# Performance work log

Hardware: AMD Instinct MI355X
Metric: run time of the kernel (lower is better)

The kernel has to match this reference:

```python
import jax, jax.numpy as jnp
import numpy as np

N = 100000      # nodes
E = 1600000     # edges
DIN = 128       # input features
H = 64          # hidden size of each of the 3 GATConv layers
EPS = 1e-16     # PyG softmax denominator epsilon


def _glorot(key, shape):
    fan_in, fan_out = shape[0], shape[-1]
    s = float(np.sqrt(6.0 / (fan_in + fan_out)))
    return jax.random.uniform(key, shape, jnp.float32, -s, s)


def setup_inputs() -> dict:
    key = jax.random.key(0)
    ks = jax.random.split(key, 18)
    x = jax.random.normal(ks[0], (N, DIN), jnp.float32)
    edge_index = jax.random.randint(ks[1], (2, E), 0, N, jnp.int32)
    dims = [(DIN, H), (H, H), (H, H)]
    params = {}
    ki = 2
    for li, (din, dout) in enumerate(dims, start=1):
        params[f"W{li}s"] = _glorot(ks[ki], (din, dout)); ki += 1
        params[f"W{li}d"] = _glorot(ks[ki], (din, dout)); ki += 1
        params[f"a{li}s"] = _glorot(ks[ki], (1, dout))[0]; ki += 1
        params[f"a{li}d"] = _glorot(ks[ki], (1, dout))[0]; ki += 1
        params[f"b{li}"] = jnp.zeros((dout,), jnp.float32)
    return dict(x=x, edge_index=edge_index, **params)


def gat_layer(x, src, dst, Ws, Wd, a_s, a_d, b):
    # single-head GATConv, negative_slope=0 -> relu on logits, no self-loops
    hs = x @ Ws                      # [N, H] source-side features (messages)
    hd = x @ Wd                      # [N, H] destination-side features
    als = hs @ a_s                   # [N] per-node source attention term
    ald = hd @ a_d                   # [N] per-node destination attention term
    logit = jax.nn.relu(als[src] + ald[dst])          # [E]
    # segment softmax over incoming edges of each destination node
    seg_max = jax.ops.segment_max(logit, dst, num_segments=N)
    ex = jnp.exp(logit - seg_max[dst])                # [E]
    denom = jax.ops.segment_sum(ex, dst, num_segments=N)
    alpha = ex / (denom[dst] + EPS)                   # [E]
    out = jax.ops.segment_sum(alpha[:, None] * hs[src], dst, num_segments=N)
    return out + b


def reference(x, edge_index,
              W1s, W1d, a1s, a1d, b1,
              W2s, W2d, a2s, a2d, b2,
              W3s, W3d, a3s, a3d, b3):
    src, dst = edge_index[0], edge_index[1]
    x = gat_layer(x, src, dst, W1s, W1d, a1s, a1d, b1)
    x = gat_layer(x, src, dst, W2s, W2d, a2s, a2d, b2)
    x = gat_layer(x, src, dst, W3s, W3d, a3s, a3d, b3)
    return x
```

## Files before the change

kernel.cpp:

```cpp
#include <hip/hip_runtime.h>
#include <hip/hip_fp16.h>

#define HDIM 64
#define EPS_F 1e-16f
#define CH 8192
#define BSH 9
#define SRCB 17

__global__ void compute_vd_all_kernel(const float* __restrict__ Wd1, const float* __restrict__ ad1,
                                      const float* __restrict__ Wd2, const float* __restrict__ ad2,
                                      const float* __restrict__ Wd3, const float* __restrict__ ad3,
                                      float* __restrict__ vd) {
    int l = blockIdx.x;
    int k = threadIdx.x;
    const float* Wd = (l == 0) ? Wd1 : (l == 1) ? Wd2 : Wd3;
    const float* ad = (l == 0) ? ad1 : (l == 1) ? ad2 : ad3;
    int din = (l == 0) ? 128 : 64;
    int off = (l == 0) ? 0 : (l == 1) ? 128 : 192;
    if (k >= din) return;
    float s = 0.f;
#pragma unroll
    for (int j = 0; j < HDIM; ++j) s = fmaf(Wd[k * HDIM + j], ad[j], s);
    vd[off + k] = s;
}

template <int DIN>
__global__ __launch_bounds__(256) void gemm_fused_kernel(
    const float* __restrict__ xin, const float* __restrict__ Ws,
    const float* __restrict__ as_, const float* __restrict__ vd,
    __half* __restrict__ hs, float* __restrict__ als, float* __restrict__ ald,
    int N) {
    __shared__ float wsh[DIN * HDIM];
    __shared__ float xs[32 * (DIN + 4)];
    __shared__ float ash[HDIM];
    __shared__ float vdsh[DIN];

    const int tid = threadIdx.x;
    const int n0 = blockIdx.x * 32;

    for (int i = tid * 4; i < DIN * HDIM; i += 256 * 4)
        *(float4*)&wsh[i] = *(const float4*)&Ws[i];
    if (tid < HDIM) ash[tid] = as_[tid];
    if (tid < DIN) vdsh[tid] = vd[tid];
    for (int i = tid; i < 32 * DIN / 4; i += 256) {
        int idx = i * 4;
        int n = idx / DIN, k = idx - n * DIN;
        float4 v = make_float4(0.f, 0.f, 0.f, 0.f);
        if (n0 + n < N) v = *(const float4*)&xin[(size_t)(n0 + n) * DIN + k];
        *(float4*)&xs[n * (DIN + 4) + k] = v;
    }
    __syncthreads();

    const int nl = tid >> 3, jg = tid & 7, j0 = jg * 8;
    const int n = n0 + nl;
    float acc[8] = {0.f, 0.f, 0.f, 0.f, 0.f, 0.f, 0.f, 0.f};
    float aldp = 0.f;
    const float* xrow = &xs[nl * (DIN + 4)];
#pragma unroll 4
    for (int k = 0; k < DIN; ++k) {
        float xv = xrow[k];
        aldp = fmaf(xv, vdsh[k], aldp);
        float4 w0 = *(const float4*)&wsh[k * HDIM + j0];
        float4 w1 = *(const float4*)&wsh[k * HDIM + j0 + 4];
        acc[0] = fmaf(xv, w0.x, acc[0]);
        acc[1] = fmaf(xv, w0.y, acc[1]);
        acc[2] = fmaf(xv, w0.z, acc[2]);
        acc[3] = fmaf(xv, w0.w, acc[3]);
        acc[4] = fmaf(xv, w1.x, acc[4]);
        acc[5] = fmaf(xv, w1.y, acc[5]);
        acc[6] = fmaf(xv, w1.z, acc[6]);
        acc[7] = fmaf(xv, w1.w, acc[7]);
    }
    float alsp = 0.f;
#pragma unroll
    for (int jj = 0; jj < 8; ++jj) alsp = fmaf(acc[jj], ash[j0 + jj], alsp);
    alsp += __shfl_down(alsp, 4, 8);
    alsp += __shfl_down(alsp, 2, 8);
    alsp += __shfl_down(alsp, 1, 8);

    if (n < N) {
        union { __half h[8]; float4 f; } u;
#pragma unroll
        for (int jj = 0; jj < 8; ++jj) u.h[jj] = __float2half_rn(acc[jj]);
        *(float4*)&hs[(size_t)n * HDIM + j0] = u.f;
        if (jg == 0) {
            als[n] = alsp;
            ald[n] = aldp;
        }
    }
}

__global__ void zero_kernel(int* __restrict__ p, int n) {
    int i = blockIdx.x * blockDim.x + threadIdx.x;
    if (i < n) p[i] = 0;
}

__global__ __launch_bounds__(256) void bucket_hist_kernel(const int* __restrict__ dst,
                                                          int* __restrict__ gbucket, int E) {
    __shared__ int bh[256];
    int t = threadIdx.x;
    bh[t] = 0;
    __syncthreads();
    int e0 = blockIdx.x * CH;
#pragma unroll
    for (int i = 0; i < CH / 256; ++i) {
        int e = e0 + i * 256 + t;
        if (e < E) atomicAdd(&bh[dst[e] >> BSH], 1);
    }
    __syncthreads();
    if (bh[t]) atomicAdd(&gbucket[t], bh[t]);
}

__global__ __launch_bounds__(256) void bucket_scan_kernel(const int* __restrict__ gbucket,
                                                          int* __restrict__ bucket_base,
                                                          int* __restrict__ bucket_cur,
                                                          int nbuk, int E) {
    __shared__ int tmp[256];
    int t = threadIdx.x;
    int v = (t < nbuk) ? gbucket[t] : 0;
    tmp[t] = v;
    __syncthreads();
    for (int off = 1; off < 256; off <<= 1) {
        int a = (t >= off) ? tmp[t - off] : 0;
        __syncthreads();
        tmp[t] += a;
        __syncthreads();
    }
    int excl = tmp[t] - v;
    if (t < nbuk) {
        bucket_base[t] = excl;
        bucket_cur[t] = excl;
    }
    if (t == 0) bucket_base[nbuk] = E;
}

__global__ __launch_bounds__(256) void bin_kernel(const int* __restrict__ src,
                                                  const int* __restrict__ dst,
                                                  int* __restrict__ bucket_cur,
                                                  unsigned int* __restrict__ epack, int E) {
    __shared__ int lcnt[256], lbase[256];
    int t = threadIdx.x;
    int e0 = blockIdx.x * CH;
    lcnt[t] = 0;
    __syncthreads();
#pragma unroll
    for (int i = 0; i < CH / 256; ++i) {
        int e = e0 + i * 256 + t;
        if (e < E) atomicAdd(&lcnt[dst[e] >> BSH], 1);
    }
    __syncthreads();
    int c = lcnt[t];
    if (c) lbase[t] = atomicAdd(&bucket_cur[t], c);
    __syncthreads();
    lcnt[t] = 0;
    __syncthreads();
#pragma unroll
    for (int i = 0; i < CH / 256; ++i) {
        int e = e0 + i * 256 + t;
        if (e < E) {
            int d = dst[e];
            int bk = d >> BSH;
            int pos = lbase[bk] + atomicAdd(&lcnt[bk], 1);
            epack[pos] = ((unsigned int)(d & 511) << SRCB) | (unsigned int)src[e];
        }
    }
}

__global__ __launch_bounds__(256) void bucket_sort_kernel(
    const unsigned int* __restrict__ epack, const int* __restrict__ bucket_base,
    int* __restrict__ rowptr, int* __restrict__ csr_src, int N, int E) {
    __shared__ int cnt[512], cur[512], psum[256];
    int b = blockIdx.x, t = threadIdx.x;
    int n0 = b << BSH;
    int nlocal = min(512, N - n0);
    int bstart = bucket_base[b], bend = bucket_base[b + 1];
    cnt[t] = 0;
    cnt[t + 256] = 0;
    __syncthreads();
    for (int k = bstart + t; k < bend; k += 256)
        atomicAdd(&cnt[epack[k] >> SRCB], 1);
    __syncthreads();
    int p = cnt[2 * t] + cnt[2 * t + 1];
    psum[t] = p;
    __syncthreads();
    for (int off = 1; off < 256; off <<= 1) {
        int a = (t >= off) ? psum[t - off] : 0;
        __syncthreads();
        psum[t] += a;
        __syncthreads();
    }
    int excl = psum[t] - p;
    int o0 = excl, o1 = excl + cnt[2 * t];
    cur[2 * t] = o0;
    cur[2 * t + 1] = o1;
    if (2 * t < nlocal) rowptr[n0 + 2 * t] = bstart + o0;
    if (2 * t + 1 < nlocal) rowptr[n0 + 2 * t + 1] = bstart + o1;
    __syncthreads();
    for (int k = bstart + t; k < bend; k += 256) {
        unsigned int e = epack[k];
        int pos = bstart + atomicAdd(&cur[e >> SRCB], 1);
        csr_src[pos] = (int)(e & ((1u << SRCB) - 1u));
    }
    if (b == 0 && t == 0) rowptr[N] = E;
}

__global__ __launch_bounds__(256) void gat_sparse_kernel(
    const int* __restrict__ rowptr, const int* __restrict__ csr_src,
    const float* __restrict__ als, const float* __restrict__ ald,
    const __half* __restrict__ hs, const float* __restrict__ b,
    float* __restrict__ out, int N) {
    int wid = (blockIdx.x * 256 + threadIdx.x) >> 6;
    int lane = threadIdx.x & 63;
    if (wid >= N) return;
    int start = rowptr[wid], end = rowptr[wid + 1];
    int deg = end - start;
    float aldd = ald[wid];

    if (deg <= 64) {
        bool valid = lane < deg;
        int s = 0;
        float ex = 0.f;
        if (valid) {
            s = csr_src[start + lane];
            float l = als[s] + aldd;
            l = l > 0.f ? l : 0.f;
            ex = __expf(l);
        }
        float denom = ex;
#pragma unroll
        for (int off = 32; off; off >>= 1) denom += __shfl_xor(denom, off);

        const int esub = lane >> 4, fg = lane & 15;
        float a0 = 0.f, a1 = 0.f, a2 = 0.f, a3 = 0.f;
        for (int k0 = 0; k0 < deg; k0 += 8) {
            int ia = k0 + esub, ib = k0 + 4 + esub;
            float exa = __shfl(ex, ia), exb = __shfl(ex, ib);
            int sa = __shfl(s, ia), sb = __shfl(s, ib);
            union { uint2 u; __half h[4]; } ra, rb;
            ra.u = *(const uint2*)&hs[(size_t)sa * HDIM + fg * 4];
            rb.u = *(const uint2*)&hs[(size_t)sb * HDIM + fg * 4];
            a0 = fmaf(exa, __half2float(ra.h[0]), a0);
            a1 = fmaf(exa, __half2float(ra.h[1]), a1);
            a2 = fmaf(exa, __half2float(ra.h[2]), a2);
            a3 = fmaf(exa, __half2float(ra.h[3]), a3);
            a0 = fmaf(exb, __half2float(rb.h[0]), a0);
            a1 = fmaf(exb, __half2float(rb.h[1]), a1);
            a2 = fmaf(exb, __half2float(rb.h[2]), a2);
            a3 = fmaf(exb, __half2float(rb.h[3]), a3);
        }
#pragma unroll
        for (int off = 16; off < 64; off <<= 1) {
            a0 += __shfl_xor(a0, off);
            a1 += __shfl_xor(a1, off);
            a2 += __shfl_xor(a2, off);
            a3 += __shfl_xor(a3, off);
        }
        if (esub == 0) {
            float inv = 1.f / (denom + EPS_F);
            const float4 b4 = *(const float4*)&b[fg * 4];
            float4 o;
            o.x = a0 * inv + b4.x;
            o.y = a1 * inv + b4.y;
            o.z = a2 * inv + b4.z;
            o.w = a3 * inv + b4.w;
            *(float4*)&out[(size_t)wid * HDIM + fg * 4] = o;
        }
        return;
    }

    float m = 0.f;
    for (int k = start + lane; k < end; k += 64)
        m = fmaxf(m, als[csr_src[k]] + aldd);
#pragma unroll
    for (int off = 32; off; off >>= 1) m = fmaxf(m, __shfl_xor(m, off));

    const int esub = lane >> 4, fg = lane & 15;
    float4 acc = make_float4(0.f, 0.f, 0.f, 0.f);
    float denom = 0.f;
    for (int k0 = start; k0 < end; k0 += 8) {
        int ka = k0 + esub, kb = k0 + 4 + esub;
        float exa = 0.f, exb = 0.f;
        uint2 ra = make_uint2(0u, 0u), rb = make_uint2(0u, 0u);
        if (ka < end) {
            int s = csr_src[ka];
            float l = als[s] + aldd;
            l = l > 0.f ? l : 0.f;
            exa = __expf(l - m);
            ra = *(const uint2*)&hs[(size_t)s * HDIM + fg * 4];
        }
        if (kb < end) {
            int s = csr_src[kb];
            float l = als[s] + aldd;
            l = l > 0.f ? l : 0.f;
            exb = __expf(l - m);
            rb = *(const uint2*)&hs[(size_t)s * HDIM + fg * 4];
        }
        denom += exa + exb;
        float2 fa0 = __half22float2(*(__half2*)&ra.x);
        float2 fa1 = __half22float2(*(__half2*)&ra.y);
        float2 fb0 = __half22float2(*(__half2*)&rb.x);
        float2 fb1 = __half22float2(*(__half2*)&rb.y);
        acc.x = fmaf(exa, fa0.x, acc.x);
        acc.y = fmaf(exa, fa0.y, acc.y);
        acc.z = fmaf(exa, fa1.x, acc.z);
        acc.w = fmaf(exa, fa1.y, acc.w);
        acc.x = fmaf(exb, fb0.x, acc.x);
        acc.y = fmaf(exb, fb0.y, acc.y);
        acc.z = fmaf(exb, fb1.x, acc.z);
        acc.w = fmaf(exb, fb1.y, acc.w);
    }
#pragma unroll
    for (int off = 16; off < 64; off <<= 1) {
        acc.x += __shfl_xor(acc.x, off);
        acc.y += __shfl_xor(acc.y, off);
        acc.z += __shfl_xor(acc.z, off);
        acc.w += __shfl_xor(acc.w, off);
        denom += __shfl_xor(denom, off);
    }
    if (esub == 0) {
        float inv = 1.f / (denom + EPS_F);
        const float4 b4 = *(const float4*)&b[fg * 4];
        float4 o;
        o.x = acc.x * inv + b4.x;
        o.y = acc.y * inv + b4.y;
        o.z = acc.z * inv + b4.z;
        o.w = acc.w * inv + b4.w;
        *(float4*)&out[(size_t)wid * HDIM + fg * 4] = o;
    }
}

extern "C" void kernel_launch(void* const* d_in, const int* in_sizes, int n_in,
                              void* d_out, int out_size, void* d_ws, size_t ws_size,
                              hipStream_t stream) {
    const float* x = (const float*)d_in[0];
    const int* ei = (const int*)d_in[1];
    const int E = in_sizes[1] / 2;
    const int din1 = in_sizes[2] / HDIM;
    const int N = in_sizes[0] / din1;
    const int* src = ei;
    const int* dst = ei + E;

    const float* P[15];
    for (int i = 0; i < 15; ++i) P[i] = (const float*)d_in[2 + i];

    float* w = (float*)d_ws;
    __half* hs = (__half*)w;  w += (size_t)N * HDIM / 2;
    float* xb = w;            w += (size_t)N * HDIM;
    float* als = w;           w += N;
    float* ald = w;           w += N;
    float* vd = w;            w += 256;
    int* ip = (int*)w;
    unsigned int* epack = (unsigned int*)ip; ip += E;
    int* csr_src = ip;        ip += E;
    int* rowptr = ip;         ip += N + 1;
    int* gbucket = ip;        ip += 256;
    int* bucket_base = ip;    ip += 257;
    int* bucket_cur = ip;     ip += 256;

    const int BT = 256;
    const int gridN32 = (N + 31) / 32;
    const int nbuk = (N + 511) >> BSH;
    const int gridCH = (E + CH - 1) / CH;
    const int gridSparse = (N * 64 + BT - 1) / BT;

    zero_kernel<<<1, 256, 0, stream>>>(gbucket, 256);
    bucket_hist_kernel<<<gridCH, BT, 0, stream>>>(dst, gbucket, E);
    bucket_scan_kernel<<<1, BT, 0, stream>>>(gbucket, bucket_base, bucket_cur, nbuk, E);
    bin_kernel<<<gridCH, BT, 0, stream>>>(src, dst, bucket_cur, epack, E);
    bucket_sort_kernel<<<nbuk, BT, 0, stream>>>(epack, bucket_base, rowptr, csr_src, N, E);

    compute_vd_all_kernel<<<3, 128, 0, stream>>>(P[1], P[3], P[6], P[8], P[11], P[13], vd);

    auto run_layer = [&](const float* xin, int din, const float* Ws, const float* vdl,
                         const float* as_, const float* b, float* xout) {
        if (din == 128)
            gemm_fused_kernel<128><<<gridN32, BT, 0, stream>>>(xin, Ws, as_, vdl, hs, als, ald, N);
        else
            gemm_fused_kernel<64><<<gridN32, BT, 0, stream>>>(xin, Ws, as_, vdl, hs, als, ald, N);
        gat_sparse_kernel<<<gridSparse, BT, 0, stream>>>(rowptr, csr_src, als, ald, hs, b,
                                                         xout, N);
    };

    float* out = (float*)d_out;
    run_layer(x,   din1, P[0],  vd,       P[2],  P[4],  xb);
    run_layer(xb,  HDIM, P[5],  vd + 128, P[7],  P[9],  out);
    run_layer(out, HDIM, P[10], vd + 192, P[12], P[14], out);
}
```

Baseline: 414.4 us.

## Use MFMA fp16 GEMM with fused attention columns and fp16 intermediate activations

The scalar FP32 dense projection is replaced by an MFMA 16x16x32 fp16 kernel. Its weight matrix is pre-transposed and gets two extra columns, Ws·a_s and Wd·a_d, so the per-node attention terms come out of the same matrix multiply. Shared memory uses XOR swizzling, and layers 1 and 2 now write hidden activations as fp16, which halves their write and read traffic. This lowers dense compute and memory cost, at the price of fp16 rounding on the inputs, the attention vectors and the intermediate activations.

```diff
diff --git a/kernel.cpp b/kernel.cpp
--- a/kernel.cpp
+++ b/kernel.cpp
@@ -7,85 +7,128 @@
 #define BSH 9
 #define SRCB 17
 
-__global__ void compute_vd_all_kernel(const float* __restrict__ Wd1, const float* __restrict__ ad1,
-                                      const float* __restrict__ Wd2, const float* __restrict__ ad2,
-                                      const float* __restrict__ Wd3, const float* __restrict__ ad3,
-                                      float* __restrict__ vd) {
-    int l = blockIdx.x;
-    int k = threadIdx.x;
-    const float* Wd = (l == 0) ? Wd1 : (l == 1) ? Wd2 : Wd3;
-    const float* ad = (l == 0) ? ad1 : (l == 1) ? ad2 : ad3;
-    int din = (l == 0) ? 128 : 64;
-    int off = (l == 0) ? 0 : (l == 1) ? 128 : 192;
-    if (k >= din) return;
-    float s = 0.f;
-#pragma unroll
-    for (int j = 0; j < HDIM; ++j) s = fmaf(Wd[k * HDIM + j], ad[j], s);
-    vd[off + k] = s;
-}
-
-template <int DIN>
-__global__ __launch_bounds__(256) void gemm_fused_kernel(
-    const float* __restrict__ xin, const float* __restrict__ Ws,
-    const float* __restrict__ as_, const float* __restrict__ vd,
-    __half* __restrict__ hs, float* __restrict__ als, float* __restrict__ ald,
-    int N) {
-    __shared__ float wsh[DIN * HDIM];
-    __shared__ float xs[32 * (DIN + 4)];
-    __shared__ float ash[HDIM];
-    __shared__ float vdsh[DIN];
-
+using half8  = __attribute__((ext_vector_type(8))) _Float16;
+using floatx4 = __attribute__((ext_vector_type(4))) float;
+
+__global__ void build_wt_kernel(const float* __restrict__ Ws, const float* __restrict__ as_,
+                                const float* __restrict__ Wd, const float* __restrict__ ad,
+                                _Float16* __restrict__ wt, int din) {
+    int tid = threadIdx.x;
+    for (int idx = tid; idx < 64 * din; idx += 256) {
+        int c = idx / din, k = idx - c * din;
+        wt[c * din + k] = (_Float16)Ws[k * 64 + c];
+    }
+    for (int k = tid; k < din; k += 256) {
+        float u = 0.f, v = 0.f;
+#pragma unroll
+        for (int j = 0; j < 64; ++j) {
+            u = fmaf(Ws[k * 64 + j], as_[j], u);
+            v = fmaf(Wd[k * 64 + j], ad[j], v);
+        }
+        wt[64 * din + k] = (_Float16)u;
+        wt[65 * din + k] = (_Float16)v;
+    }
+    for (int idx = tid; idx < 14 * din; idx += 256) wt[66 * din + idx] = (_Float16)0.f;
+}
+
+template <int DIN, bool F32IN>
+__global__ __launch_bounds__(256) void gemm_mfma_kernel(
+    const void* __restrict__ xin, const _Float16* __restrict__ wt,
+    _Float16* __restrict__ hs, float* __restrict__ als, float* __restrict__ ald, int N) {
+    constexpr int KB = DIN / 8;
+    __shared__ _Float16 xs[64 * DIN];
+    __shared__ _Float16 ws[80 * DIN];
     const int tid = threadIdx.x;
-    const int n0 = blockIdx.x * 32;
-
-    for (int i = tid * 4; i < DIN * HDIM; i += 256 * 4)
-        *(float4*)&wsh[i] = *(const float4*)&Ws[i];
-    if (tid < HDIM) ash[tid] = as_[tid];
-    if (tid < DIN) vdsh[tid] = vd[tid];
-    for (int i = tid; i < 32 * DIN / 4; i += 256) {
-        int idx = i * 4;
-        int n = idx / DIN, k = idx - n * DIN;
-        float4 v = make_float4(0.f, 0.f, 0.f, 0.f);
-        if (n0 + n < N) v = *(const float4*)&xin[(size_t)(n0 + n) * DIN + k];
-        *(float4*)&xs[n * (DIN + 4) + k] = v;
-    }
-    __syncthreads();
-
-    const int nl = tid >> 3, jg = tid & 7, j0 = jg * 8;
-    const int n = n0 + nl;
-    float acc[8] = {0.f, 0.f, 0.f, 0.f, 0.f, 0.f, 0.f, 0.f};
-    float aldp = 0.f;
-    const float* xrow = &xs[nl * (DIN + 4)];
-#pragma unroll 4
-    for (int k = 0; k < DIN; ++k) {
-        float xv = xrow[k];
-        aldp = fmaf(xv, vdsh[k], aldp);
-        float4 w0 = *(const float4*)&wsh[k * HDIM + j0];
-        float4 w1 = *(const float4*)&wsh[k * HDIM + j0 + 4];
-        acc[0] = fmaf(xv, w0.x, acc[0]);
-        acc[1] = fmaf(xv, w0.y, acc[1]);
-        acc[2] = fmaf(xv, w0.z, acc[2]);
-        acc[3] = fmaf(xv, w0.w, acc[3]);
-        acc[4] = fmaf(xv, w1.x, acc[4]);
-        acc[5] = fmaf(xv, w1.y, acc[5]);
-        acc[6] = fmaf(xv, w1.z, acc[6]);
-        acc[7] = fmaf(xv, w1.w, acc[7]);
-    }
-    float alsp = 0.f;
-#pragma unroll
-    for (int jj = 0; jj < 8; ++jj) alsp = fmaf(acc[jj], ash[j0 + jj], alsp);
-    alsp += __shfl_down(alsp, 4, 8);
-    alsp += __shfl_down(alsp, 2, 8);
-    alsp += __shfl_down(alsp, 1, 8);
-
-    if (n < N) {
-        union { __half h[8]; float4 f; } u;
-#pragma unroll
-        for (int jj = 0; jj < 8; ++jj) u.h[jj] = __float2half_rn(acc[jj]);
-        *(float4*)&hs[(size_t)n * HDIM + j0] = u.f;
-        if (jg == 0) {
-            als[n] = alsp;
-            ald[n] = aldp;
+    const int n0 = blockIdx.x * 64;
+
+    for (int c = tid; c < 80 * KB; c += 256) {
+        int row = c / KB, kb = c - row * KB;
+        half8 v = *(const half8*)&wt[row * DIN + kb * 8];
+        *(half8*)&ws[row * DIN + ((kb ^ (row & 7)) * 8)] = v;
+    }
+    if (F32IN) {
+        const float* xf = (const float*)xin;
+        for (int c = tid; c < 64 * KB; c += 256) {
+            int row = c / KB, kb = c - row * KB;
+            int n = n0 + row;
+            half8 v;
+#pragma unroll
+            for (int j = 0; j < 8; ++j) v[j] = (_Float16)0.f;
+            if (n < N) {
+                const float* p = &xf[(size_t)n * DIN + kb * 8];
+                float4 f0 = *(const float4*)p;
+                float4 f1 = *(const float4*)(p + 4);
+                v[0] = (_Float16)f0.x; v[1] = (_Float16)f0.y;
+                v[2] = (_Float16)f0.z; v[3] = (_Float16)f0.w;
+                v[4] = (_Float16)f1.x; v[5] = (_Float16)f1.y;
+                v[6] = (_Float16)f1.z; v[7] = (_Float16)f1.w;
+            }
+            *(half8*)&xs[row * DIN + ((kb ^ (row & 7)) * 8)] = v;
+        }
+    } else {
+        const _Float16* xh = (const _Float16*)xin;
+        for (int c = tid; c < 64 * KB; c += 256) {
+            int row = c / KB, kb = c - row * KB;
+            int n = n0 + row;
+            half8 v;
+#pragma unroll
+            for (int j = 0; j < 8; ++j) v[j] = (_Float16)0.f;
+            if (n < N) v = *(const half8*)&xh[(size_t)n * DIN + kb * 8];
+            *(half8*)&xs[row * DIN + ((kb ^ (row & 7)) * 8)] = v;
+        }
+    }
+    __syncthreads();
+
+    const int lane = tid & 63, wave = tid >> 6;
+    const int r16 = lane & 15, kg = lane >> 4;
+    const int arow = wave * 16 + r16;
+
+    floatx4 acc[5];
+#pragma unroll
+    for (int t = 0; t < 5; ++t)
+#pragma unroll
+        for (int r = 0; r < 4; ++r) acc[t][r] = 0.f;
+
+#pragma unroll
+    for (int ks = 0; ks < DIN / 32; ++ks) {
+        int kbb = ks * 4 + kg;
+        half8 a = *(const half8*)&xs[arow * DIN + ((kbb ^ (arow & 7)) * 8)];
+        int bswz = (kbb ^ (r16 & 7)) * 8;
+        half8 b0 = *(const half8*)&ws[(r16)*DIN + bswz];
+        half8 b1 = *(const half8*)&ws[(16 + r16) * DIN + bswz];
+        half8 b2 = *(const half8*)&ws[(32 + r16) * DIN + bswz];
+        half8 b3 = *(const half8*)&ws[(48 + r16) * DIN + bswz];
+        half8 b4 = *(const half8*)&ws[(64 + r16) * DIN + bswz];
+        acc[0] = __builtin_amdgcn_mfma_f32_16x16x32_f16(a, b0, acc[0], 0, 0, 0);
+        acc[1] = __builtin_amdgcn_mfma_f32_16x16x32_f16(a, b1, acc[1], 0, 0, 0);
+        acc[2] = __builtin_amdgcn_mfma_f32_16x16x32_f16(a, b2, acc[2], 0, 0, 0);
+        acc[3] = __builtin_amdgcn_mfma_f32_16x16x32_f16(a, b3, acc[3], 0, 0, 0);
+        acc[4] = __builtin_amdgcn_mfma_f32_16x16x32_f16(a, b4, acc[4], 0, 0, 0);
+    }
+
+    __syncthreads();
+    constexpr int OS = 72;
+    _Float16* os = ws;
+#pragma unroll
+    for (int t = 0; t < 4; ++t)
+#pragma unroll
+        for (int r = 0; r < 4; ++r) {
+            int row = wave * 16 + kg * 4 + r;
+            os[row * OS + t * 16 + r16] = (_Float16)acc[t][r];
+        }
+    __syncthreads();
+    for (int c = tid; c < 64 * 8; c += 256) {
+        int row = c >> 3, kb = c & 7;
+        int n = n0 + row;
+        if (n < N)
+            *(half8*)&hs[(size_t)n * HDIM + kb * 8] = *(const half8*)&os[row * OS + kb * 8];
+    }
+    if (r16 < 2) {
+        float* dst = (r16 == 0) ? als : ald;
+#pragma unroll
+        for (int r = 0; r < 4; ++r) {
+            int n = n0 + wave * 16 + kg * 4 + r;
+            if (n < N) dst[n] = acc[4][r];
         }
     }
 }
@@ -204,11 +247,12 @@
     if (b == 0 && t == 0) rowptr[N] = E;
 }
 
+template <bool F32OUT>
 __global__ __launch_bounds__(256) void gat_sparse_kernel(
     const int* __restrict__ rowptr, const int* __restrict__ csr_src,
     const float* __restrict__ als, const float* __restrict__ ald,
     const __half* __restrict__ hs, const float* __restrict__ b,
-    float* __restrict__ out, int N) {
+    float* __restrict__ out, _Float16* __restrict__ outh, int N) {
     int wid = (blockIdx.x * 256 + threadIdx.x) >> 6;
     int lane = threadIdx.x & 63;
     if (wid >= N) return;
@@ -258,12 +302,16 @@
         if (esub == 0) {
             float inv = 1.f / (denom + EPS_F);
             const float4 b4 = *(const float4*)&b[fg * 4];
-            float4 o;
-            o.x = a0 * inv + b4.x;
-            o.y = a1 * inv + b4.y;
-            o.z = a2 * inv + b4.z;
-            o.w = a3 * inv + b4.w;
-            *(float4*)&out[(size_t)wid * HDIM + fg * 4] = o;
+            float o0 = a0 * inv + b4.x, o1 = a1 * inv + b4.y;
+            float o2 = a2 * inv + b4.z, o3 = a3 * inv + b4.w;
+            if (F32OUT) {
+                *(float4*)&out[(size_t)wid * HDIM + fg * 4] = make_float4(o0, o1, o2, o3);
+            } else {
+                union { _Float16 h[4]; uint2 u; } ov;
+                ov.h[0] = (_Float16)o0; ov.h[1] = (_Float16)o1;
+                ov.h[2] = (_Float16)o2; ov.h[3] = (_Float16)o3;
+                *(uint2*)&outh[(size_t)wid * HDIM + fg * 4] = ov.u;
+            }
         }
         return;
     }
@@ -320,12 +368,16 @@
     if (esub == 0) {
         float inv = 1.f / (denom + EPS_F);
         const float4 b4 = *(const float4*)&b[fg * 4];
-        float4 o;
-        o.x = acc.x * inv + b4.x;
-        o.y = acc.y * inv + b4.y;
-        o.z = acc.z * inv + b4.z;
-        o.w = acc.w * inv + b4.w;
-        *(float4*)&out[(size_t)wid * HDIM + fg * 4] = o;
+        float o0 = acc.x * inv + b4.x, o1 = acc.y * inv + b4.y;
+        float o2 = acc.z * inv + b4.z, o3 = acc.w * inv + b4.w;
+        if (F32OUT) {
+            *(float4*)&out[(size_t)wid * HDIM + fg * 4] = make_float4(o0, o1, o2, o3);
+        } else {
+            union { _Float16 h[4]; uint2 u; } ov;
+            ov.h[0] = (_Float16)o0; ov.h[1] = (_Float16)o1;
+            ov.h[2] = (_Float16)o2; ov.h[3] = (_Float16)o3;
+            *(uint2*)&outh[(size_t)wid * HDIM + fg * 4] = ov.u;
+        }
     }
 }
 
@@ -343,22 +395,25 @@
     const float* P[15];
     for (int i = 0; i < 15; ++i) P[i] = (const float*)d_in[2 + i];
 
-    float* w = (float*)d_ws;
-    __half* hs = (__half*)w;  w += (size_t)N * HDIM / 2;
-    float* xb = w;            w += (size_t)N * HDIM;
-    float* als = w;           w += N;
-    float* ald = w;           w += N;
-    float* vd = w;            w += 256;
-    int* ip = (int*)w;
+    _Float16* hp = (_Float16*)d_ws;
+    _Float16* hs = hp;   hp += (size_t)N * HDIM;
+    _Float16* xh = hp;   hp += (size_t)N * HDIM;
+    _Float16* wt1 = hp;  hp += 80 * 128;
+    _Float16* wt2 = hp;  hp += 80 * 64;
+    _Float16* wt3 = hp;  hp += 80 * 64;
+    float* fp = (float*)hp;
+    float* als = fp;     fp += N;
+    float* ald = fp;     fp += N;
+    int* ip = (int*)fp;
     unsigned int* epack = (unsigned int*)ip; ip += E;
-    int* csr_src = ip;        ip += E;
-    int* rowptr = ip;         ip += N + 1;
-    int* gbucket = ip;        ip += 256;
-    int* bucket_base = ip;    ip += 257;
-    int* bucket_cur = ip;     ip += 256;
+    int* csr_src = ip;   ip += E;
+    int* rowptr = ip;    ip += N + 1;
+    int* gbucket = ip;   ip += 256;
+    int* bucket_base = ip; ip += 257;
+    int* bucket_cur = ip;  ip += 256;
 
     const int BT = 256;
-    const int gridN32 = (N + 31) / 32;
+    const int gridG = (N + 63) / 64;
     const int nbuk = (N + 511) >> BSH;
     const int gridCH = (E + CH - 1) / CH;
     const int gridSparse = (N * 64 + BT - 1) / BT;
@@ -369,20 +424,22 @@
     bin_kernel<<<gridCH, BT, 0, stream>>>(src, dst, bucket_cur, epack, E);
     bucket_sort_kernel<<<nbuk, BT, 0, stream>>>(epack, bucket_base, rowptr, csr_src, N, E);
 
-    compute_vd_all_kernel<<<3, 128, 0, stream>>>(P[1], P[3], P[6], P[8], P[11], P[13], vd);
-
-    auto run_layer = [&](const float* xin, int din, const float* Ws, const float* vdl,
-                         const float* as_, const float* b, float* xout) {
-        if (din == 128)
-            gemm_fused_kernel<128><<<gridN32, BT, 0, stream>>>(xin, Ws, as_, vdl, hs, als, ald, N);
-        else
-            gemm_fused_kernel<64><<<gridN32, BT, 0, stream>>>(xin, Ws, as_, vdl, hs, als, ald, N);
-        gat_sparse_kernel<<<gridSparse, BT, 0, stream>>>(rowptr, csr_src, als, ald, hs, b,
-                                                         xout, N);
-    };
+    build_wt_kernel<<<1, 256, 0, stream>>>(P[0], P[2], P[1], P[3], wt1, 128);
+    build_wt_kernel<<<1, 256, 0, stream>>>(P[5], P[7], P[6], P[8], wt2, 64);
+    build_wt_kernel<<<1, 256, 0, stream>>>(P[10], P[12], P[11], P[13], wt3, 64);
 
     float* out = (float*)d_out;
-    run_layer(x,   din1, P[0],  vd,       P[2],  P[4],  xb);
-    run_layer(xb,  HDIM, P[5],  vd + 128, P[7],  P[9],  out);
-    run_layer(out, HDIM, P[10], vd + 192, P[12], P[14], out);
-}
+
+    gemm_mfma_kernel<128, true><<<gridG, BT, 0, stream>>>(x, wt1, hs, als, ald, N);
+    gat_sparse_kernel<false><<<gridSparse, BT, 0, stream>>>(rowptr, csr_src, als, ald,
+                                                            (const __half*)hs, P[4],
+                                                            nullptr, xh, N);
+    gemm_mfma_kernel<64, false><<<gridG, BT, 0, stream>>>(xh, wt2, hs, als, ald, N);
+    gat_sparse_kernel<false><<<gridSparse, BT, 0, stream>>>(rowptr, csr_src, als, ald,
+                                                            (const __half*)hs, P[9],
+                                                            nullptr, xh, N);
+    gemm_mfma_kernel<64, false><<<gridG, BT, 0, stream>>>(xh, wt3, hs, als, ald, N);
+    gat_sparse_kernel<true><<<gridSparse, BT, 0, stream>>>(rowptr, csr_src, als, ald,
+                                                           (const __half*)hs, P[14],
+                                                           out, nullptr, N);
+}
```

Result: faster. 380.2 us (-8.2%).
